# Performance work log

Measured on AMD Instinct MI355X. Metric: run time of the kernel, lower is better.

Reference implementation:

```python
import jax, jax.numpy as jnp
import numpy as np
from jax import lax

B, L, D_IN, H, RES, BD, D_OUT = 1024, 128, 5, 64, 256, 8, 1


def setup_inputs() -> dict:
    key = jax.random.key(0)
    ks = jax.random.split(key, 14)
    f = jnp.float32
    d = {}
    d["V_noise"] = jax.random.normal(ks[0], (B, D_IN), f)
    d["increments"] = jax.random.normal(ks[1], (B, L, BD), f)
    d["W1"] = jax.random.normal(ks[2], (H, D_IN), f) / np.float32(np.sqrt(D_IN))
    d["b1"] = jnp.zeros((H,), f)
    d["W2"] = jax.random.normal(ks[3], (RES, H), f) / np.float32(np.sqrt(H))
    d["b2"] = jnp.zeros((RES,), f)
    d["rho1"] = jax.random.normal(ks[4], (1, 1), f)
    d["rho2"] = jax.random.normal(ks[5], (1, 1), f)
    d["rho3"] = jax.random.normal(ks[6], (1, 1), f)
    d["rho4"] = jax.random.normal(ks[7], (1, 1), f)
    d["rho5"] = jax.random.normal(ks[8], (1, 1), f)
    # scale reservoir matrices by 1/sqrt(res) so pre-activations are O(1)
    d["B1"] = jax.random.normal(ks[9], (RES, RES), f) / np.float32(np.sqrt(RES))
    d["B2"] = jax.random.normal(ks[10], (BD, RES, RES), f) / np.float32(np.sqrt(RES))
    d["lambda1"] = jax.random.normal(ks[11], (RES, 1), f)
    d["lambda2"] = jax.random.normal(ks[12], (BD, RES, 1), f)
    d["Wr"] = jax.random.normal(ks[13], (D_OUT, RES), f) / np.float32(np.sqrt(RES))
    d["br"] = jnp.zeros((D_OUT,), f)
    return d


def reference(V_noise, increments, W1, b1, W2, b2,
              rho1, rho2, rho3, rho4, rho5,
              B1, B2, lambda1, lambda2, Wr, br):
    act = jnp.tanh
    # initial-condition MLP: [B, D_in] -> [B, RES]
    V = act(V_noise @ W1.T + b1) @ W2.T + b2
    # Brownian path with W[:,0] = 0
    Wp = jnp.cumsum(increments, axis=1).at[:, 0, :].set(0.0)
    dW = Wp[:, 1:] - Wp[:, :-1]          # [B, L-1, BD]
    l1 = lambda1[:, 0]                    # [RES]
    l2 = lambda2[:, :, 0]                 # [BD, RES]
    rho5s = rho5[0, 0]

    def step(r, dw):                      # r: [B, RES], dw: [B, BD]
        drift = act(rho1 * (r @ B1.T) + rho2 * l1)                      # [B, RES]
        diff = act(rho3 * jnp.einsum('kij,bj->bki', B2, r) + rho4 * l2)  # [B, BD, RES]
        rn = r + drift + rho5s * jnp.einsum('bki,bk->bi', diff, dw)
        return rn, rn

    _, Rs = lax.scan(step, V, jnp.swapaxes(dW, 0, 1))  # [L-1, B, RES]
    Rall = jnp.concatenate([V[None], Rs], axis=0)       # [L, B, RES]
    # time-homogeneous linear readout per lag, concatenated along time
    x = Rall @ Wr.T + br                                 # [L, B, D_out]
    out = jnp.transpose(x, (1, 0, 2)).reshape(V.shape[0], Rall.shape[0] * x.shape[-1], 1)
    return out
```

## Files before the change

kernel.cpp:

```cpp
#include <hip/hip_runtime.h>
#include <hip/hip_bf16.h>

#define B_TOT 1024
#define L_T   128
#define DIN   5
#define HD    64
#define RESN  256
#define BDN   8
#define NMAT  9
#define NROWS (NMAT * RESN)
#define PLANE ((size_t)NROWS * RESN)
#define NGRP  16
#define BG    64
#define FPB   16
#define NTHR  256
#define RB_GRP_BYTES (2 * 16 * 2 * BG * FPB * 2)
#define GRP_SHORTS (RB_GRP_BYTES / 2)
#define BUF_SHORTS 32768
#define WS_RB_OFF  (2 * PLANE * 2)
#define WS_FLAG_OFF (WS_RB_OFF + (size_t)NGRP * RB_GRP_BYTES)
#define FLAGS_PER_GRP 1024

typedef __attribute__((ext_vector_type(8))) short bf16x8;
typedef __attribute__((ext_vector_type(4))) float f32x4;
typedef __attribute__((ext_vector_type(4))) unsigned u32x4;

__device__ __forceinline__ float fast_tanh(float x) {
    float e = __expf(2.0f * x);
    return 1.0f - 2.0f * __builtin_amdgcn_rcpf(e + 1.0f);
}

__device__ __forceinline__ void split_hl(float v, unsigned short& h, unsigned short& l) {
    __hip_bfloat16 hb = __float2bfloat16(v);
    h = __builtin_bit_cast(unsigned short, hb);
    l = __builtin_bit_cast(unsigned short, __float2bfloat16(v - __bfloat162float(hb)));
}

__device__ __forceinline__ unsigned mall_load1(const unsigned* p) {
    unsigned r;
    asm volatile("global_load_dword %0, %1, off sc0 sc1" : "=v"(r) : "v"(p));
    return r;
}
__device__ __forceinline__ unsigned l2_load1(const unsigned* p) {
    unsigned r;
    asm volatile("global_load_dword %0, %1, off sc0" : "=v"(r) : "v"(p));
    return r;
}
__device__ __forceinline__ void mall_store1(unsigned* p, unsigned v) {
    asm volatile("global_store_dword %0, %1, off sc0 sc1" :: "v"(p), "v"(v) : "memory");
}
__device__ __forceinline__ u32x4 mall_load4s(const unsigned short* p) {
    u32x4 r;
    asm volatile("global_load_dwordx4 %0, %1, off sc0 sc1" : "=v"(r) : "v"(p));
    return r;
}
__device__ __forceinline__ u32x4 l2_load4s(const unsigned short* p) {
    u32x4 r;
    asm volatile("global_load_dwordx4 %0, %1, off sc0" : "=v"(r) : "v"(p));
    return r;
}
__device__ __forceinline__ void mall_store4(unsigned short* p, u32x4 v) {
    asm volatile("global_store_dwordx4 %0, %1, off sc0 sc1" :: "v"(p), "v"(v) : "memory");
}
__device__ __forceinline__ void l2_store4(unsigned short* p, u32x4 v) {
    asm volatile("global_store_dwordx4 %0, %1, off sc0" :: "v"(p), "v"(v) : "memory");
}
__device__ __forceinline__ void atom_add_l2(unsigned* p, unsigned v) {
    asm volatile("global_atomic_add %0, %1, off" :: "v"(p), "v"(v) : "memory");
}
__device__ __forceinline__ void atom_addf_l2(float* p, float v) {
    asm volatile("global_atomic_add_f32 %0, %1, off" :: "v"(p), "v"(v) : "memory");
}
__device__ __forceinline__ void wait_vm0() {
    asm volatile("s_waitcnt vmcnt(0)" ::: "memory");
}
__device__ __forceinline__ void wait_lgkm0() {
    asm volatile("s_waitcnt lgkmcnt(0)" ::: "memory");
}

__device__ __forceinline__ void spin_all(const unsigned* fladdr, unsigned want, bool l2m) {
    unsigned guard = 0;
    for (;;) {
        unsigned fv = l2m ? l2_load1(fladdr) : mall_load1(fladdr);
        wait_vm0();
        if (__ballot(fv < want) == 0ull) break;
        __builtin_amdgcn_s_sleep(1);
        if (++guard > (1u << 20)) break;
    }
}

__global__ void conv_w(const float* __restrict__ B1, const float* __restrict__ B2,
                       __hip_bfloat16* __restrict__ wh, __hip_bfloat16* __restrict__ wl) {
    int idx = blockIdx.x * 256 + threadIdx.x;
    float v = (idx < RESN * RESN) ? B1[idx] : B2[idx - RESN * RESN];
    __hip_bfloat16 h = __float2bfloat16(v);
    wh[idx] = h;
    wl[idx] = __float2bfloat16(v - __bfloat162float(h));
}

__global__ __launch_bounds__(NTHR, 1) void sde_ws(
    const float* __restrict__ Vn,  const float* __restrict__ inc,
    const float* __restrict__ W1,  const float* __restrict__ b1,
    const float* __restrict__ W2,  const float* __restrict__ b2,
    const float* __restrict__ rho1p, const float* __restrict__ rho2p,
    const float* __restrict__ rho3p, const float* __restrict__ rho4p,
    const float* __restrict__ rho5p,
    const float* __restrict__ lam1, const float* __restrict__ lam2,
    const float* __restrict__ Wr,  const float* __restrict__ brp,
    const __hip_bfloat16* __restrict__ wbf,
    unsigned short* __restrict__ rbs,
    unsigned int* __restrict__ flags,
    float* __restrict__ out)
{
    __shared__ __align__(16) short wlds[2][NMAT][8][64][8];
    __shared__ __align__(16) unsigned short stage[4][512];
    __shared__ int l2mode_sh;

    const int tid  = threadIdx.x;
    const int mt   = tid >> 6;
    const int lane = tid & 63;
    const int n16  = lane & 15;
    const int quad = lane >> 4;
    const int bx   = blockIdx.x;
    const int g    = ((bx & 7) << 1) | (bx >> 7);
    const int fb   = (bx >> 3) & 15;
    const int f0   = fb * FPB;
    const int b0g  = g * BG;
    unsigned short* gbs = rbs + (size_t)g * GRP_SHORTS;
    unsigned int* flagp  = flags + g * FLAGS_PER_GRP;
    unsigned int* myflag = flagp + (fb * 4 + mt) * 16;
    const unsigned* fladdr = (const unsigned*)(flagp + ((lane & 15) * 4 + mt) * 16);
    unsigned* regtbl = flags + NGRP * FLAGS_PER_GRP;
    unsigned* regcnt = regtbl + 256;

    if (tid == 0) {
        unsigned xcd;
        asm volatile("s_getreg_b32 %0, hwreg(HW_REG_XCC_ID)" : "=s"(xcd));
        mall_store1(&regtbl[bx], xcd);
        wait_vm0();
        __hip_atomic_fetch_add(regcnt, 1u, __ATOMIC_RELAXED, __HIP_MEMORY_SCOPE_AGENT);
    }

    const float rho1 = rho1p[0], rho2 = rho2p[0], rho3 = rho3p[0],
                rho4 = rho4p[0], rho5 = rho5p[0];
    const float brv = brp[0];
    const float bradd = (fb == 0) ? brv : 0.0f;

    float* hf  = (float*)&wlds[0][0][0][0][0];
    float* vsh = hf + 64 * 66;
    for (int p = tid; p < BG * HD; p += NTHR) {
        int b = p >> 6, hh = p & 63;
        float s = b1[hh];
        #pragma unroll
        for (int d = 0; d < DIN; ++d) s += Vn[(b0g + b) * DIN + d] * W1[hh * DIN + d];
        hf[b * 66 + hh] = fast_tanh(s);
    }
    __syncthreads();

    if (tid == 0) {
        unsigned cnt, guard = 0;
        do {
            cnt = mall_load1(regcnt);
            wait_vm0();
            if (cnt >= 256) break;
            __builtin_amdgcn_s_sleep(1);
        } while (++guard < (1u << 22));
        unsigned e[16];
        #pragma unroll
        for (int q = 0; q < 16; ++q)
            e[q] = mall_load1(&regtbl[((g & 1) << 7) | (q << 3) | (g >> 1)]);
        wait_vm0();
        int ok = (cnt >= 256) ? 1 : 0;
        #pragma unroll
        for (int q = 1; q < 16; ++q) ok &= (e[q] == e[0]) ? 1 : 0;
        l2mode_sh = ok;
    }
    __syncthreads();
    const bool l2m = (l2mode_sh != 0);

    {
        int bl = lane >> 2;
        int b  = 16 * mt + bl;
        #pragma unroll
        for (int i = 0; i < 4; ++i) {
            int f = (lane & 3) * 4 + i;
            float s = b2[f0 + f];
            #pragma unroll 8
            for (int hh = 0; hh < HD; ++hh) s += hf[b * 66 + hh] * W2[(f0 + f) * HD + hh];
            vsh[b * 16 + f] = s;
            unsigned short h_, l_;
            split_hl(s, h_, l_);
            stage[mt][0 * 256 + bl * 16 + f] = h_;
            stage[mt][1 * 256 + bl * 16 + f] = l_;
        }
        wait_lgkm0();
        u32x4 v = *(const u32x4*)&stage[mt][lane * 8];
        unsigned short* dst = gbs + 0 * BUF_SHORTS + fb * 2048 +
                              (lane >> 5) * 1024 + 16 * mt * 16 + (lane & 31) * 8;
        if (l2m) l2_store4(dst, v); else mall_store4(dst, v);
    }
    wait_vm0();
    if (lane == 0) {
        if (l2m) atom_add_l2(myflag, 1u);
        else __hip_atomic_fetch_add(myflag, 1u, __ATOMIC_RELAXED, __HIP_MEMORY_SCOPE_AGENT);
    }

    float rmast[4];
    #pragma unroll
    for (int rg = 0; rg < 4; ++rg) rmast[rg] = vsh[(16 * mt + 4 * quad + rg) * 16 + n16];
    const float l1c = lam1[f0 + n16];
    const float wrv = Wr[f0 + n16];
    float l2c[BDN];
    #pragma unroll
    for (int k = 0; k < BDN; ++k) l2c[k] = lam2[k * RESN + f0 + n16];
    __syncthreads();

    for (int e = tid; e < 2 * NMAT * 8 * 64; e += NTHR) {
        int l  = e & 63;
        int kk = (e >> 6) & 7;
        int m  = e >> 9;
        int pl = (m >= NMAT) ? 1 : 0;
        int nt = m - pl * NMAT;
        const uint4* src = (const uint4*)(wbf + (size_t)pl * PLANE +
            (size_t)(nt * RESN + f0 + (l & 15)) * RESN + kk * 32 + (l >> 4) * 8);
        *(uint4*)&wlds[pl][nt][kk][l][0] = *src;
    }
    __syncthreads();

    const unsigned short* pcb = gbs + (quad >> 1) * 2048 + (16 * mt + n16) * 16 + (quad & 1) * 8;

    for (int t = 0; t < L_T; ++t) {
        {
            float po[4];
            #pragma unroll
            for (int rg = 0; rg < 4; ++rg) {
                float p = wrv * rmast[rg];
                p += __shfl_xor(p, 1);
                p += __shfl_xor(p, 2);
                p += __shfl_xor(p, 4);
                p += __shfl_xor(p, 8);
                po[rg] = p;
            }
            if (n16 == 0) {
                #pragma unroll
                for (int rg = 0; rg < 4; ++rg) {
                    float* op = out + (size_t)(b0g + 16 * mt + 4 * quad + rg) * L_T + t;
                    float v = po[rg] + bradd;
                    if (l2m) atom_addf_l2(op, v);
                    else __hip_atomic_fetch_add(op, v, __ATOMIC_RELAXED, __HIP_MEMORY_SCOPE_AGENT);
                }
            }
        }
        if (t == L_T - 1) break;

        float dwv[4][8];
        #pragma unroll
        for (int rg = 0; rg < 4; ++rg) {
            const size_t bglob = (size_t)(b0g + 16 * mt + 4 * quad + rg) * (L_T * BDN);
            const float4 d0 = *(const float4*)(inc + bglob + (size_t)(t + 1) * BDN);
            const float4 d1 = *(const float4*)(inc + bglob + (size_t)(t + 1) * BDN + 4);
            dwv[rg][0] = d0.x; dwv[rg][1] = d0.y; dwv[rg][2] = d0.z; dwv[rg][3] = d0.w;
            dwv[rg][4] = d1.x; dwv[rg][5] = d1.y; dwv[rg][6] = d1.z; dwv[rg][7] = d1.w;
            if (t == 0) {
                const float4 e0 = *(const float4*)(inc + bglob);
                const float4 e1 = *(const float4*)(inc + bglob + 4);
                dwv[rg][0] += e0.x; dwv[rg][1] += e0.y; dwv[rg][2] += e0.z; dwv[rg][3] += e0.w;
                dwv[rg][4] += e1.x; dwv[rg][5] += e1.y; dwv[rg][6] += e1.z; dwv[rg][7] += e1.w;
            }
        }
        spin_all(fladdr, (unsigned)(t + 1), l2m);
        const int cur = t & 1, nxt = cur ^ 1;

        bf16x8 afh[8], afl[8];
        {
            const unsigned short* pc = pcb + cur * BUF_SHORTS;
            if (l2m) {
                #pragma unroll
                for (int kk = 0; kk < 8; ++kk) {
                    afh[kk] = __builtin_bit_cast(bf16x8, l2_load4s(pc + kk * 4096));
                    afl[kk] = __builtin_bit_cast(bf16x8, l2_load4s(pc + kk * 4096 + 1024));
                }
            } else {
                #pragma unroll
                for (int kk = 0; kk < 8; ++kk) {
                    afh[kk] = __builtin_bit_cast(bf16x8, mall_load4s(pc + kk * 4096));
                    afl[kk] = __builtin_bit_cast(bf16x8, mall_load4s(pc + kk * 4096 + 1024));
                }
            }
        }
        wait_vm0();

        f32x4 acc[NMAT] = {};
        #pragma unroll
        for (int kk = 0; kk < 8; ++kk) {
            bf16x8 bh[NMAT], bl[NMAT];
            #pragma unroll
            for (int nt = 0; nt < NMAT; ++nt) {
                bh[nt] = *(const bf16x8*)&wlds[0][nt][kk][lane][0];
                bl[nt] = *(const bf16x8*)&wlds[1][nt][kk][lane][0];
            }
            #pragma unroll
            for (int nt = 0; nt < NMAT; ++nt)
                acc[nt] = __builtin_amdgcn_mfma_f32_16x16x32_bf16(afh[kk], bh[nt], acc[nt], 0, 0, 0);
            #pragma unroll
            for (int nt = 0; nt < NMAT; ++nt)
                acc[nt] = __builtin_amdgcn_mfma_f32_16x16x32_bf16(afl[kk], bh[nt], acc[nt], 0, 0, 0);
            #pragma unroll
            for (int nt = 0; nt < NMAT; ++nt)
                acc[nt] = __builtin_amdgcn_mfma_f32_16x16x32_bf16(afh[kk], bl[nt], acc[nt], 0, 0, 0);
        }

        #pragma unroll
        for (int rg = 0; rg < 4; ++rg) {
            float drift = fast_tanh(rho1 * acc[0][rg] + rho2 * l1c);
            float s = 0.0f;
            #pragma unroll
            for (int k = 0; k < BDN; ++k)
                s += fast_tanh(rho3 * acc[1 + k][rg] + rho4 * l2c[k]) * dwv[rg][k];
            float rn = rmast[rg] + drift + rho5 * s;
            rmast[rg] = rn;
            unsigned short h_, l_;
            split_hl(rn, h_, l_);
            stage[mt][0 * 256 + (4 * quad + rg) * 16 + n16] = h_;
            stage[mt][1 * 256 + (4 * quad + rg) * 16 + n16] = l_;
        }
        wait_lgkm0();
        {
            u32x4 v = *(const u32x4*)&stage[mt][lane * 8];
            unsigned short* dst = gbs + nxt * BUF_SHORTS + fb * 2048 +
                                  (lane >> 5) * 1024 + 16 * mt * 16 + (lane & 31) * 8;
            if (l2m) l2_store4(dst, v); else mall_store4(dst, v);
        }
        wait_vm0();
        if (lane == 0) {
            if (l2m) atom_add_l2(myflag, 1u);
            else __hip_atomic_fetch_add(myflag, 1u, __ATOMIC_RELAXED, __HIP_MEMORY_SCOPE_AGENT);
        }
    }
}

extern "C" void kernel_launch(void* const* d_in, const int* in_sizes, int n_in,
                              void* d_out, int out_size, void* d_ws, size_t ws_size,
                              hipStream_t stream) {
    const float* Vn   = (const float*)d_in[0];
    const float* inc  = (const float*)d_in[1];
    const float* W1   = (const float*)d_in[2];
    const float* b1   = (const float*)d_in[3];
    const float* W2   = (const float*)d_in[4];
    const float* b2   = (const float*)d_in[5];
    const float* r1   = (const float*)d_in[6];
    const float* r2   = (const float*)d_in[7];
    const float* r3   = (const float*)d_in[8];
    const float* r4   = (const float*)d_in[9];
    const float* r5   = (const float*)d_in[10];
    const float* B1   = (const float*)d_in[11];
    const float* B2   = (const float*)d_in[12];
    const float* lam1 = (const float*)d_in[13];
    const float* lam2 = (const float*)d_in[14];
    const float* Wr   = (const float*)d_in[15];
    const float* br   = (const float*)d_in[16];

    __hip_bfloat16* wh    = (__hip_bfloat16*)d_ws;
    unsigned short* rbs   = (unsigned short*)((char*)d_ws + WS_RB_OFF);
    unsigned int*   flags = (unsigned int*)((char*)d_ws + WS_FLAG_OFF);
    float* out = (float*)d_out;

    hipMemsetAsync(d_out, 0, out_size, stream);
    hipMemsetAsync(flags, 0, NGRP * FLAGS_PER_GRP * sizeof(unsigned int) + 2048, stream);
    conv_w<<<dim3(NROWS * RESN / 256), dim3(256), 0, stream>>>(B1, B2, wh, wh + PLANE);
    sde_ws<<<dim3(256), dim3(NTHR), 0, stream>>>(
        Vn, inc, W1, b1, W2, b2, r1, r2, r3, r4, r5, lam1, lam2, Wr, br,
        wh, rbs, flags, out);
}
```

Baseline: 770.8 us.

## Repartition SDE workgroups to 8 features per block with 8 waves and paired matrix tiles

Changes the decomposition from 16 batch groups of 64 rows with 16 features per block to 8 groups of 128 rows with 8 features per block, using 8 waves per block and allowing 2 blocks per CU. Matrix tiles now pack two reservoir matrices per 16-column MFMA tile (5 tiles instead of 9), and the two half-results are combined with a lane shuffle. Per-step flag signalling uses plain stores of the step counter instead of atomic adds. This aims to cut redundant MFMA work and LDS weight footprint per block and to spread the cross-block synchronisation differently, at the cost of more flags to poll per wave (32 instead of 16) and larger exchange buffers.

```diff
diff --git a/kernel.cpp b/kernel.cpp
--- a/kernel.cpp
+++ b/kernel.cpp
@@ -10,16 +10,16 @@
 #define NMAT  9
 #define NROWS (NMAT * RESN)
 #define PLANE ((size_t)NROWS * RESN)
-#define NGRP  16
-#define BG    64
-#define FPB   16
-#define NTHR  256
-#define RB_GRP_BYTES (2 * 16 * 2 * BG * FPB * 2)
-#define GRP_SHORTS (RB_GRP_BYTES / 2)
-#define BUF_SHORTS 32768
+#define NGRP  8
+#define BG    128
+#define FPB   8
+#define NW    8
+#define NTHR  (NW * 64)
+#define BUF_SHORTS 65536
+#define RB_GRP_BYTES (2 * BUF_SHORTS * 2)
 #define WS_RB_OFF  (2 * PLANE * 2)
 #define WS_FLAG_OFF (WS_RB_OFF + (size_t)NGRP * RB_GRP_BYTES)
-#define FLAGS_PER_GRP 1024
+#define FLAGS_PER_GRP 4096
 
 typedef __attribute__((ext_vector_type(8))) short bf16x8;
 typedef __attribute__((ext_vector_type(4))) float f32x4;
@@ -49,6 +49,9 @@
 __device__ __forceinline__ void mall_store1(unsigned* p, unsigned v) {
     asm volatile("global_store_dword %0, %1, off sc0 sc1" :: "v"(p), "v"(v) : "memory");
 }
+__device__ __forceinline__ void l2_store1(unsigned* p, unsigned v) {
+    asm volatile("global_store_dword %0, %1, off sc0" :: "v"(p), "v"(v) : "memory");
+}
 __device__ __forceinline__ u32x4 mall_load4s(const unsigned short* p) {
     u32x4 r;
     asm volatile("global_load_dwordx4 %0, %1, off sc0 sc1" : "=v"(r) : "v"(p));
@@ -64,9 +67,6 @@
 }
 __device__ __forceinline__ void l2_store4(unsigned short* p, u32x4 v) {
     asm volatile("global_store_dwordx4 %0, %1, off sc0" :: "v"(p), "v"(v) : "memory");
-}
-__device__ __forceinline__ void atom_add_l2(unsigned* p, unsigned v) {
-    asm volatile("global_atomic_add %0, %1, off" :: "v"(p), "v"(v) : "memory");
 }
 __device__ __forceinline__ void atom_addf_l2(float* p, float v) {
     asm volatile("global_atomic_add_f32 %0, %1, off" :: "v"(p), "v"(v) : "memory");
@@ -98,7 +98,7 @@
     wl[idx] = __float2bfloat16(v - __bfloat162float(h));
 }
 
-__global__ __launch_bounds__(NTHR, 1) void sde_ws(
+__global__ __launch_bounds__(NTHR, 2) void sde_ws(
     const float* __restrict__ Vn,  const float* __restrict__ inc,
     const float* __restrict__ W1,  const float* __restrict__ b1,
     const float* __restrict__ W2,  const float* __restrict__ b2,
@@ -112,8 +112,8 @@
     unsigned int* __restrict__ flags,
     float* __restrict__ out)
 {
-    __shared__ __align__(16) short wlds[2][NMAT][8][64][8];
-    __shared__ __align__(16) unsigned short stage[4][512];
+    __shared__ __align__(16) short wlds[2][5][8][64][8];
+    __shared__ __align__(16) unsigned short stage[NW][256];
     __shared__ int l2mode_sh;
 
     const int tid  = threadIdx.x;
@@ -121,15 +121,17 @@
     const int lane = tid & 63;
     const int n16  = lane & 15;
     const int quad = lane >> 4;
+    const int fl   = n16 & 7;
+    const int h    = n16 >> 3;
     const int bx   = blockIdx.x;
-    const int g    = ((bx & 7) << 1) | (bx >> 7);
-    const int fb   = (bx >> 3) & 15;
+    const int g    = bx & 7;
+    const int fb   = bx >> 3;
     const int f0   = fb * FPB;
     const int b0g  = g * BG;
-    unsigned short* gbs = rbs + (size_t)g * GRP_SHORTS;
+    unsigned short* gbs = rbs + (size_t)g * (RB_GRP_BYTES / 2);
     unsigned int* flagp  = flags + g * FLAGS_PER_GRP;
-    unsigned int* myflag = flagp + (fb * 4 + mt) * 16;
-    const unsigned* fladdr = (const unsigned*)(flagp + ((lane & 15) * 4 + mt) * 16);
+    unsigned int* myflag = flagp + (fb * NW + mt) * 16;
+    const unsigned* fladdr = (const unsigned*)(flagp + ((lane & 31) * NW + mt) * 16);
     unsigned* regtbl = flags + NGRP * FLAGS_PER_GRP;
     unsigned* regcnt = regtbl + 256;
 
@@ -147,7 +149,7 @@
     const float bradd = (fb == 0) ? brv : 0.0f;
 
     float* hf  = (float*)&wlds[0][0][0][0][0];
-    float* vsh = hf + 64 * 66;
+    float* vsh = hf + 128 * 66;
     for (int p = tid; p < BG * HD; p += NTHR) {
         int b = p >> 6, hh = p & 63;
         float s = b1[hh];
@@ -165,69 +167,79 @@
             if (cnt >= 256) break;
             __builtin_amdgcn_s_sleep(1);
         } while (++guard < (1u << 22));
-        unsigned e[16];
-        #pragma unroll
-        for (int q = 0; q < 16; ++q)
-            e[q] = mall_load1(&regtbl[((g & 1) << 7) | (q << 3) | (g >> 1)]);
+        unsigned e[32];
+        #pragma unroll
+        for (int q = 0; q < 32; ++q) {
+            e[q] = mall_load1(&regtbl[g + (q << 3)]);
+        }
         wait_vm0();
         int ok = (cnt >= 256) ? 1 : 0;
         #pragma unroll
-        for (int q = 1; q < 16; ++q) ok &= (e[q] == e[0]) ? 1 : 0;
+        for (int q = 1; q < 32; ++q) ok &= (e[q] == e[0]) ? 1 : 0;
         l2mode_sh = ok;
+    }
+
+    for (int p = tid; p < BG * FPB; p += NTHR) {
+        int b = p >> 3, f = p & 7;
+        float s = b2[f0 + f];
+        #pragma unroll 8
+        for (int hh = 0; hh < HD; ++hh) s += hf[b * 66 + hh] * W2[(f0 + f) * HD + hh];
+        vsh[b * 8 + f] = s;
     }
     __syncthreads();
     const bool l2m = (l2mode_sh != 0);
 
-    {
-        int bl = lane >> 2;
-        int b  = 16 * mt + bl;
-        #pragma unroll
-        for (int i = 0; i < 4; ++i) {
-            int f = (lane & 3) * 4 + i;
-            float s = b2[f0 + f];
-            #pragma unroll 8
-            for (int hh = 0; hh < HD; ++hh) s += hf[b * 66 + hh] * W2[(f0 + f) * HD + hh];
-            vsh[b * 16 + f] = s;
+    float rmast[4];
+    #pragma unroll
+    for (int rg = 0; rg < 4; ++rg) {
+        float v = vsh[(16 * mt + 4 * quad + rg) * 8 + fl];
+        rmast[rg] = v;
+        if (h == 0) {
             unsigned short h_, l_;
-            split_hl(s, h_, l_);
-            stage[mt][0 * 256 + bl * 16 + f] = h_;
-            stage[mt][1 * 256 + bl * 16 + f] = l_;
-        }
-        wait_lgkm0();
+            split_hl(v, h_, l_);
+            stage[mt][0 * 128 + (4 * quad + rg) * 8 + fl] = h_;
+            stage[mt][1 * 128 + (4 * quad + rg) * 8 + fl] = l_;
+        }
+    }
+    wait_lgkm0();
+    if (lane < 32) {
         u32x4 v = *(const u32x4*)&stage[mt][lane * 8];
-        unsigned short* dst = gbs + 0 * BUF_SHORTS + fb * 2048 +
-                              (lane >> 5) * 1024 + 16 * mt * 16 + (lane & 31) * 8;
+        unsigned short* dst = gbs + 0 * BUF_SHORTS + fb * 2048 + mt * 256 + lane * 8;
         if (l2m) l2_store4(dst, v); else mall_store4(dst, v);
     }
     wait_vm0();
     if (lane == 0) {
-        if (l2m) atom_add_l2(myflag, 1u);
-        else __hip_atomic_fetch_add(myflag, 1u, __ATOMIC_RELAXED, __HIP_MEMORY_SCOPE_AGENT);
-    }
-
-    float rmast[4];
+        if (l2m) l2_store1(myflag, 1u); else mall_store1(myflag, 1u);
+    }
+
+    const float l1c = lam1[f0 + fl];
+    const float wrv = (n16 < 8) ? Wr[f0 + n16] : 0.0f;
+    float l2v[5];
     #pragma unroll
-    for (int rg = 0; rg < 4; ++rg) rmast[rg] = vsh[(16 * mt + 4 * quad + rg) * 16 + n16];
-    const float l1c = lam1[f0 + n16];
-    const float wrv = Wr[f0 + n16];
-    float l2c[BDN];
-    #pragma unroll
-    for (int k = 0; k < BDN; ++k) l2c[k] = lam2[k * RESN + f0 + n16];
+    for (int tt = 0; tt < 5; ++tt) {
+        int k = 2 * tt - 1 + h;
+        l2v[tt] = (k >= 0 && k < 8) ? lam2[k * RESN + f0 + fl] : 0.0f;
+    }
     __syncthreads();
 
-    for (int e = tid; e < 2 * NMAT * 8 * 64; e += NTHR) {
+    for (int e = tid; e < 2 * 5 * 8 * 64; e += NTHR) {
         int l  = e & 63;
         int kk = (e >> 6) & 7;
-        int m  = e >> 9;
-        int pl = (m >= NMAT) ? 1 : 0;
-        int nt = m - pl * NMAT;
-        const uint4* src = (const uint4*)(wbf + (size_t)pl * PLANE +
-            (size_t)(nt * RESN + f0 + (l & 15)) * RESN + kk * 32 + (l >> 4) * 8);
-        *(uint4*)&wlds[pl][nt][kk][l][0] = *src;
+        int rem = e >> 9;
+        int pl = (rem >= 5) ? 1 : 0;
+        int tt = rem - pl * 5;
+        int m  = 2 * tt + ((l >> 3) & 1);
+        uint4 v = make_uint4(0, 0, 0, 0);
+        if (m < NMAT) {
+            const uint4* src = (const uint4*)(wbf + (size_t)pl * PLANE +
+                (size_t)(m * RESN + f0 + (l & 7)) * RESN + kk * 32 + (l >> 4) * 8);
+            v = *src;
+        }
+        *(uint4*)&wlds[pl][tt][kk][l][0] = v;
     }
     __syncthreads();
 
-    const unsigned short* pcb = gbs + (quad >> 1) * 2048 + (16 * mt + n16) * 16 + (quad & 1) * 8;
+    const unsigned short* pcb = gbs + quad * 2048 + mt * 256 + n16 * 8;
 
     for (int t = 0; t < L_T; ++t) {
         {
@@ -277,64 +289,73 @@
             if (l2m) {
                 #pragma unroll
                 for (int kk = 0; kk < 8; ++kk) {
-                    afh[kk] = __builtin_bit_cast(bf16x8, l2_load4s(pc + kk * 4096));
-                    afl[kk] = __builtin_bit_cast(bf16x8, l2_load4s(pc + kk * 4096 + 1024));
+                    afh[kk] = __builtin_bit_cast(bf16x8, l2_load4s(pc + kk * 8192));
+                    afl[kk] = __builtin_bit_cast(bf16x8, l2_load4s(pc + kk * 8192 + 128));
                 }
             } else {
                 #pragma unroll
                 for (int kk = 0; kk < 8; ++kk) {
-                    afh[kk] = __builtin_bit_cast(bf16x8, mall_load4s(pc + kk * 4096));
-                    afl[kk] = __builtin_bit_cast(bf16x8, mall_load4s(pc + kk * 4096 + 1024));
+                    afh[kk] = __builtin_bit_cast(bf16x8, mall_load4s(pc + kk * 8192));
+                    afl[kk] = __builtin_bit_cast(bf16x8, mall_load4s(pc + kk * 8192 + 128));
                 }
             }
         }
         wait_vm0();
 
-        f32x4 acc[NMAT] = {};
+        f32x4 acc[5] = {};
         #pragma unroll
         for (int kk = 0; kk < 8; ++kk) {
-            bf16x8 bh[NMAT], bl[NMAT];
-            #pragma unroll
-            for (int nt = 0; nt < NMAT; ++nt) {
-                bh[nt] = *(const bf16x8*)&wlds[0][nt][kk][lane][0];
-                bl[nt] = *(const bf16x8*)&wlds[1][nt][kk][lane][0];
-            }
-            #pragma unroll
-            for (int nt = 0; nt < NMAT; ++nt)
-                acc[nt] = __builtin_amdgcn_mfma_f32_16x16x32_bf16(afh[kk], bh[nt], acc[nt], 0, 0, 0);
-            #pragma unroll
-            for (int nt = 0; nt < NMAT; ++nt)
-                acc[nt] = __builtin_amdgcn_mfma_f32_16x16x32_bf16(afl[kk], bh[nt], acc[nt], 0, 0, 0);
-            #pragma unroll
-            for (int nt = 0; nt < NMAT; ++nt)
-                acc[nt] = __builtin_amdgcn_mfma_f32_16x16x32_bf16(afh[kk], bl[nt], acc[nt], 0, 0, 0);
+            bf16x8 bh[5], bl[5];
+            #pragma unroll
+            for (int tt = 0; tt < 5; ++tt) {
+                bh[tt] = *(const bf16x8*)&wlds[0][tt][kk][lane][0];
+                bl[tt] = *(const bf16x8*)&wlds[1][tt][kk][lane][0];
+            }
+            #pragma unroll
+            for (int tt = 0; tt < 5; ++tt)
+                acc[tt] = __builtin_amdgcn_mfma_f32_16x16x32_bf16(afh[kk], bh[tt], acc[tt], 0, 0, 0);
+            #pragma unroll
+            for (int tt = 0; tt < 5; ++tt)
+                acc[tt] = __builtin_amdgcn_mfma_f32_16x16x32_bf16(afl[kk], bh[tt], acc[tt], 0, 0, 0);
+            #pragma unroll
+            for (int tt = 0; tt < 5; ++tt)
+                acc[tt] = __builtin_amdgcn_mfma_f32_16x16x32_bf16(afh[kk], bl[tt], acc[tt], 0, 0, 0);
         }
 
         #pragma unroll
         for (int rg = 0; rg < 4; ++rg) {
-            float drift = fast_tanh(rho1 * acc[0][rg] + rho2 * l1c);
-            float s = 0.0f;
-            #pragma unroll
-            for (int k = 0; k < BDN; ++k)
-                s += fast_tanh(rho3 * acc[1 + k][rg] + rho4 * l2c[k]) * dwv[rg][k];
-            float rn = rmast[rg] + drift + rho5 * s;
+            float p;
+            if (h == 0) {
+                p  = fast_tanh(rho1 * acc[0][rg] + rho2 * l1c);
+                p += rho5 * fast_tanh(rho3 * acc[1][rg] + rho4 * l2v[1]) * dwv[rg][1];
+                p += rho5 * fast_tanh(rho3 * acc[2][rg] + rho4 * l2v[2]) * dwv[rg][3];
+                p += rho5 * fast_tanh(rho3 * acc[3][rg] + rho4 * l2v[3]) * dwv[rg][5];
+                p += rho5 * fast_tanh(rho3 * acc[4][rg] + rho4 * l2v[4]) * dwv[rg][7];
+            } else {
+                p  = rho5 * fast_tanh(rho3 * acc[0][rg] + rho4 * l2v[0]) * dwv[rg][0];
+                p += rho5 * fast_tanh(rho3 * acc[1][rg] + rho4 * l2v[1]) * dwv[rg][2];
+                p += rho5 * fast_tanh(rho3 * acc[2][rg] + rho4 * l2v[2]) * dwv[rg][4];
+                p += rho5 * fast_tanh(rho3 * acc[3][rg] + rho4 * l2v[3]) * dwv[rg][6];
+            }
+            float rn = rmast[rg] + p + __shfl_xor(p, 8);
             rmast[rg] = rn;
-            unsigned short h_, l_;
-            split_hl(rn, h_, l_);
-            stage[mt][0 * 256 + (4 * quad + rg) * 16 + n16] = h_;
-            stage[mt][1 * 256 + (4 * quad + rg) * 16 + n16] = l_;
+            if (h == 0) {
+                unsigned short h_, l_;
+                split_hl(rn, h_, l_);
+                stage[mt][0 * 128 + (4 * quad + rg) * 8 + fl] = h_;
+                stage[mt][1 * 128 + (4 * quad + rg) * 8 + fl] = l_;
+            }
         }
         wait_lgkm0();
-        {
+        if (lane < 32) {
             u32x4 v = *(const u32x4*)&stage[mt][lane * 8];
-            unsigned short* dst = gbs + nxt * BUF_SHORTS + fb * 2048 +
-                                  (lane >> 5) * 1024 + 16 * mt * 16 + (lane & 31) * 8;
+            unsigned short* dst = gbs + nxt * BUF_SHORTS + fb * 2048 + mt * 256 + lane * 8;
             if (l2m) l2_store4(dst, v); else mall_store4(dst, v);
         }
         wait_vm0();
         if (lane == 0) {
-            if (l2m) atom_add_l2(myflag, 1u);
-            else __hip_atomic_fetch_add(myflag, 1u, __ATOMIC_RELAXED, __HIP_MEMORY_SCOPE_AGENT);
+            if (l2m) l2_store1(myflag, (unsigned)(t + 2));
+            else mall_store1(myflag, (unsigned)(t + 2));
         }
     }
 }
```

After: 1.109 ms. +43.9%, slower.
